# Kernel optimization log

Hardware: AMD Instinct MI355X
Metric: run time of the kernel (lower is better)

## Reference

```python
import jax, jax.numpy as jnp
import numpy as np

B, N, L = 512, 64, 64
D = 256          # item_embed_size / hidden_size
H = 256          # linear_hidden_size
V = 100000       # item_size
STEP = 1


def _p(key, shape, std=0.0625):
    return jax.random.uniform(key, shape, jnp.float32, -std, std)


def setup_inputs() -> dict:
    key = jax.random.key(0)
    ks = jax.random.split(key, 32)
    inp = {
        "alias_inputs": jax.random.randint(ks[0], (B, L), 0, N),
        "A": jax.random.uniform(ks[1], (B, N, 2 * N), jnp.float32),
        "items": jax.random.randint(ks[2], (B, N), 0, V),
        "mask": jnp.ones((B, L), jnp.int32),
        # parameters (stored as [in, out]; torch Linear applies x @ W.T + b)
        "emb": _p(ks[3], (V, D)),
        "W_ein": _p(ks[4], (D, D)), "b_ein": _p(ks[5], (D,)),
        "W_eout": _p(ks[6], (D, D)), "b_eout": _p(ks[7], (D,)),
        "b_iah": _p(ks[8], (D,)), "b_oah": _p(ks[9], (D,)),
        "W_i": _p(ks[10], (2 * D, 3 * D)), "b_i": _p(ks[11], (3 * D,)),
        "W_h": _p(ks[12], (D, 3 * D)), "b_h": _p(ks[13], (3 * D,)),
        "W1": _p(ks[14], (D, D)), "b1": _p(ks[15], (D,)),
        "W2": _p(ks[16], (D, D)), "b2": _p(ks[17], (D,)),
        "W3": _p(ks[18], (D, 1)),
        "Wn1": _p(ks[19], (2 * D, H)), "bn1": _p(ks[20], (H,)),
        "Wn2": _p(ks[21], (H, D)), "bn2": _p(ks[22], (D,)),
    }
    return inp


def reference(alias_inputs, A, items, mask,
              emb, W_ein, b_ein, W_eout, b_eout, b_iah, b_oah,
              W_i, b_i, W_h, b_h, W1, b1, W2, b2, W3, Wn1, bn1, Wn2, bn2):
    n = A.shape[1]
    hidden = emb[items]  # [B, N, D] (dropout is identity at eval)

    def gnn_cell(h):
        inp_in = jnp.matmul(A[:, :, :n], h @ W_ein + b_ein) + b_iah
        inp_out = jnp.matmul(A[:, :, n:2 * n], h @ W_eout + b_eout) + b_oah
        inputs = jnp.concatenate([inp_in, inp_out], axis=2)     # [B, N, 2D]
        gi = inputs @ W_i + b_i                                  # [B, N, 3D]
        gh = h @ W_h + b_h                                       # [B, N, 3D]
        i_r, i_i, i_n = jnp.split(gi, 3, axis=2)
        h_r, h_i, h_n = jnp.split(gh, 3, axis=2)
        resetgate = jax.nn.sigmoid(i_r + h_r)
        inputgate = jax.nn.sigmoid(i_i + h_i)
        newgate = jnp.tanh(i_n + resetgate * h_n)
        return newgate + inputgate * (h - newgate)

    for _ in range(STEP):
        hidden = gnn_cell(hidden)

    # per-sample gather of node states into sequence order
    seq_hidden = jnp.take_along_axis(hidden, alias_inputs[:, :, None], axis=1)  # [B, L, D]
    last = jnp.sum(mask, axis=1) - 1
    ht = seq_hidden[jnp.arange(seq_hidden.shape[0]), last]        # [B, D]

    q1 = (ht @ W1 + b1)[:, None, :]                               # [B, 1, D]
    q2 = seq_hidden @ W2 + b2                                     # [B, L, D]
    alpha = jax.nn.sigmoid(q1 + q2) @ W3                          # [B, L, 1]
    a = jnp.sum(alpha * seq_hidden * mask[:, :, None].astype(jnp.float32), axis=1)  # [B, D]

    x = jnp.concatenate([a, ht], axis=1)                          # [B, 2D]
    return jax.nn.relu(x @ Wn1 + bn1) @ Wn2 + bn2                 # [B, D]
```

## Files before the change

kernel.cpp:

```cpp
#include <hip/hip_runtime.h>
#include <hip/hip_bf16.h>
#include <math.h>

typedef short bhalf8 __attribute__((ext_vector_type(8)));
typedef float floatx4 __attribute__((ext_vector_type(4)));

__device__ __forceinline__ float sigmoidf_(float x) { return 1.0f / (1.0f + __expf(-x)); }

__device__ __forceinline__ unsigned short f2bf(float f) {
    unsigned int u = __builtin_bit_cast(unsigned int, f);
    u += 0x7FFFu + ((u >> 16) & 1u);
    return (unsigned short)(u >> 16);
}
__device__ __forceinline__ float bf2f(unsigned short h) {
    unsigned int u = ((unsigned int)h) << 16;
    return __builtin_bit_cast(float, u);
}

__device__ __forceinline__ floatx4 mfma16(bhalf8 a, bhalf8 b, floatx4 c) {
    return __builtin_amdgcn_mfma_f32_16x16x32_bf16(a, b, c, 0, 0, 0);
}

__device__ __forceinline__ void gl_lds16(const unsigned short* g, unsigned short* l) {
    __builtin_amdgcn_global_load_lds(
        (const __attribute__((address_space(1))) void*)g,
        (__attribute__((address_space(3))) void*)l, 16, 0, 0);
}

__device__ __forceinline__ void pack_generic(
    int b, int tid, const float* __restrict__ W0, const float* __restrict__ W1,
    int split, int N, int BN, unsigned short* __restrict__ out)
{
    int t = b * 256 + tid;
    int j = t & 7;
    int lane = (t >> 3) & 63;
    int FT = BN >> 4;
    int f = (t >> 9) % FT;
    int rest = t / (512 * FT);
    int NT = N / BN;
    int nt = rest % NT;
    int kt = rest / NT;
    int k = kt * 32 + (lane >> 4) * 8 + j;
    int n = nt * BN + f * 16 + (lane & 15);
    float v = (n < split) ? W0[(size_t)k * split + n]
                          : W1[(size_t)k * (N - split) + (n - split)];
    out[t] = f2bf(v);
}

__device__ __forceinline__ void pack_gru_(
    int b, int tid, const float* __restrict__ Wi, const float* __restrict__ Wh,
    unsigned short* __restrict__ out)
{
    int t = b * 256 + tid;
    int j = t & 7;
    int lane = (t >> 3) & 63;
    int f = (t >> 9) & 3;
    int q = t >> 11;
    int g = q % 3;
    int p = q / 3;
    int dt = p & 3;
    int kt = p >> 2;
    int k = kt * 32 + (lane >> 4) * 8 + j;
    int n = g * 256 + dt * 64 + f * 16 + (lane & 15);
    float v = (k < 512) ? Wi[(size_t)k * 768 + n] : Wh[(size_t)(k - 512) * 768 + n];
    out[t] = f2bf(v);
}

__global__ __launch_bounds__(256) void pack_all(
    const float* __restrict__ W_ein, const float* __restrict__ W_eout,
    const float* __restrict__ Wi, const float* __restrict__ Wh,
    const float* __restrict__ W2, const float* __restrict__ Wn1,
    const float* __restrict__ Wn2,
    unsigned short* __restrict__ Wio_pk, unsigned short* __restrict__ Wg_pk,
    unsigned short* __restrict__ W2pk, unsigned short* __restrict__ Wn1pk,
    unsigned short* __restrict__ Wn2pk)
{
    int bx = blockIdx.x;
    int tid = threadIdx.x;
    if (bx < 512)       pack_generic(bx,        tid, W_ein, W_eout, 256, 512, 128, Wio_pk);
    else if (bx < 2816) pack_gru_   (bx - 512,  tid, Wi, Wh, Wg_pk);
    else if (bx < 3072) pack_generic(bx - 2816, tid, W2,  W2,  256, 256, 256, W2pk);
    else if (bx < 3584) pack_generic(bx - 3072, tid, Wn1, Wn1, 256, 256, 256, Wn1pk);
    else                pack_generic(bx - 3584, tid, Wn2, Wn2, 256, 256, 256, Wn2pk);
}

__global__ __launch_bounds__(256) void gather_emb(
    const int* __restrict__ items, const float* __restrict__ emb,
    unsigned short* __restrict__ hidden_pk)
{
    int i = blockIdx.x * 256 + threadIdx.x;
    int mg = i >> 9;
    int rem = i & 511;
    int l = rem & 63;
    int m = mg * 16 + (l & 15);
    int k = (rem >> 6) * 32 + (l >> 4) * 8;
    int it = items[m];
    const float* src = emb + (size_t)it * 256 + k;
    float4 v0 = *(const float4*)src;
    float4 v1 = *(const float4*)(src + 4);
    uint4 o;
    o.x = f2bf(v0.x) | ((unsigned)f2bf(v0.y) << 16);
    o.y = f2bf(v0.z) | ((unsigned)f2bf(v0.w) << 16);
    o.z = f2bf(v1.x) | ((unsigned)f2bf(v1.y) << 16);
    o.w = f2bf(v1.z) | ((unsigned)f2bf(v1.w) << 16);
    *(uint4*)(hidden_pk + (size_t)i * 8) = o;
}

__global__ __launch_bounds__(256) void gemm_hioadj(
    const unsigned short* __restrict__ hidden_pk,
    const unsigned short* __restrict__ Wio_pk,
    const float* __restrict__ bein, const float* __restrict__ beout,
    const float* __restrict__ A,
    const float* __restrict__ biah, const float* __restrict__ boah,
    unsigned short* __restrict__ inp_pk)
{
    __shared__ unsigned short SM[24576];
    unsigned short* As0 = SM;
    unsigned short* Bs0 = SM + 8192;
    unsigned short* Hb  = SM;
    unsigned short* Ab  = SM + 16384;

    const int tid = threadIdx.x;
    const int wid = tid >> 6, lane = tid & 63;
    const int wr = wid >> 1, wc = wid & 1;
    const int bm = blockIdx.x * 128;
    const int nt = blockIdx.y;
    const int mg0 = bm >> 4;
    const int b0 = blockIdx.x * 2;
    const int half = nt >> 1;

    auto stage = [&](int kt, int buf) {
        #pragma unroll
        for (int u = 0; u < 2; ++u) {
            int rg = wid * 2 + u;
            gl_lds16(hidden_pk + ((size_t)(mg0 + rg) * 8 + kt) * 512 + lane * 8,
                     &As0[buf * 4096 + rg * 512]);
            gl_lds16(Wio_pk + ((size_t)(kt * 4 + nt) * 8 + rg) * 512 + lane * 8,
                     &Bs0[buf * 4096 + rg * 512]);
        }
    };

    floatx4 acc[4][4] = {};
    stage(0, 0);
    __syncthreads();
    #pragma unroll
    for (int kt = 0; kt < 8; ++kt) {
        int cur = kt & 1;
        if (kt < 7) stage(kt + 1, cur ^ 1);
        bhalf8 a[4], b[4];
        #pragma unroll
        for (int i = 0; i < 4; i++) a[i] = *(const bhalf8*)&As0[cur * 4096 + (wr * 4 + i) * 512 + lane * 8];
        #pragma unroll
        for (int j = 0; j < 4; j++) b[j] = *(const bhalf8*)&Bs0[cur * 4096 + (wc * 4 + j) * 512 + lane * 8];
        #pragma unroll
        for (int i = 0; i < 4; i++)
            #pragma unroll
            for (int j = 0; j < 4; j++) acc[i][j] = mfma16(a[i], b[j], acc[i][j]);
        __syncthreads();
    }
    const int r0 = (lane >> 4) * 4;
    {
        const float* bio = half ? beout : bein;
        #pragma unroll
        for (int mf = 0; mf < 4; mf++) {
            #pragma unroll
            for (int nf = 0; nf < 4; nf++) {
                int nl = wc * 64 + nf * 16 + (lane & 15);
                float bias = bio[(nt & 1) * 128 + nl];
                int base = (((wr * 2 + (mf >> 1)) * 8 + (nl >> 4)) * 64
                            + ((mf & 1) * 2 + (r0 >> 3)) * 16 + (lane & 15)) * 8 + (r0 & 7);
                ushort4 o;
                o.x = f2bf(acc[mf][nf][0] + bias);
                o.y = f2bf(acc[mf][nf][1] + bias);
                o.z = f2bf(acc[mf][nf][2] + bias);
                o.w = f2bf(acc[mf][nf][3] + bias);
                *(ushort4*)&Hb[base] = o;
            }
        }
    }
    {
        int r = tid >> 2, jj = tid & 3;
        #pragma unroll
        for (int bb = 0; bb < 2; ++bb)
            #pragma unroll
            for (int kt2 = 0; kt2 < 2; ++kt2) {
                const float* src = A + (size_t)(b0 + bb) * 8192 + r * 128 + half * 64 + kt2 * 32 + jj * 8;
                float4 v0 = *(const float4*)src;
                float4 v1 = *(const float4*)(src + 4);
                uint4 o;
                o.x = f2bf(v0.x) | ((unsigned)f2bf(v0.y) << 16);
                o.y = f2bf(v0.z) | ((unsigned)f2bf(v0.w) << 16);
                o.z = f2bf(v1.x) | ((unsigned)f2bf(v1.y) << 16);
                o.w = f2bf(v1.z) | ((unsigned)f2bf(v1.w) << 16);
                *(uint4*)&Ab[(bb * 2 + kt2) * 2048 + ((r >> 4) * 64 + jj * 16 + (r & 15)) * 8] = o;
            }
    }
    __syncthreads();
    const int bb = wid >> 1, ch = wid & 1;
    floatx4 acc2[4][4] = {};
    #pragma unroll
    for (int kt2 = 0; kt2 < 2; ++kt2) {
        bhalf8 a2[4];
        #pragma unroll
        for (int i = 0; i < 4; i++)
            a2[i] = *(const bhalf8*)&Ab[(bb * 2 + kt2) * 2048 + (i * 64 + lane) * 8];
        #pragma unroll
        for (int jf = 0; jf < 4; jf++) {
            bhalf8 bv = *(const bhalf8*)&Hb[((bb * 2 + kt2) * 8 + ch * 4 + jf) * 512 + lane * 8];
            #pragma unroll
            for (int i = 0; i < 4; i++) acc2[i][jf] = mfma16(a2[i], bv, acc2[i][jf]);
        }
    }
    {
        const float* bia = half ? boah : biah;
        const int b = b0 + bb;
        #pragma unroll
        for (int i = 0; i < 4; i++) {
            #pragma unroll
            for (int jf = 0; jf < 4; jf++) {
                int colp = (nt & 1) * 128 + (ch * 4 + jf) * 16 + (lane & 15);
                float bv = bia[colp];
                int kt5 = nt * 4 + ch * 2 + (jf >> 1);
                int l2 = ((jf & 1) * 2 + ((lane >> 3) & 1)) * 16;
                #pragma unroll
                for (int reg = 0; reg < 4; reg++) {
                    int mlo = r0 + reg;
                    size_t dst = (((size_t)(b * 4 + i) * 16 + kt5) * 64 + l2 + mlo) * 8 + (lane & 7);
                    inp_pk[dst] = f2bf(acc2[i][jf][reg] + bv);
                }
            }
        }
    }
}

__global__ __launch_bounds__(256) void gru_mfma(
    const unsigned short* __restrict__ inp_pk,
    const unsigned short* __restrict__ hidden_pk,
    const unsigned short* __restrict__ Wg_pk,
    const float* __restrict__ bi, const float* __restrict__ bh,
    unsigned short* __restrict__ newh_bf)
{
    __shared__ unsigned short As3[3][4096];
    __shared__ unsigned short Bs2[2][6144];
    const int tid = threadIdx.x;
    const int wid = tid >> 6, lane = tid & 63;
    const int wr = wid >> 1, wc = wid & 1;
    const int bm = blockIdx.x * 128;
    const int dt = blockIdx.y;
    const int mg0 = bm >> 4;

    floatx4 R[4][2] = {}, I[4][2] = {}, N0[4][2] = {}, N1[4][2] = {};

    auto stageA = [&](int st, int buf) {
        #pragma unroll
        for (int u = 0; u < 2; ++u) {
            int rg = wid * 2 + u;
            const unsigned short* src = (st < 16)
                ? inp_pk    + ((size_t)(mg0 + rg) * 16 + st) * 512
                : hidden_pk + ((size_t)(mg0 + rg) * 8 + (st - 16)) * 512;
            gl_lds16(src + lane * 8, &As3[buf][rg * 512]);
        }
    };
    auto stageB = [&](int st, int buf) {
        #pragma unroll
        for (int u = 0; u < 3; ++u) {
            int sg = wid * 3 + u;
            gl_lds16(Wg_pk + ((size_t)(st * 4 + dt) * 12 + sg) * 512 + lane * 8,
                     &Bs2[buf][sg * 512]);
        }
    };

    stageA(0, 0);
    stageB(0, 0);
    stageA(1, 1);
    #pragma unroll
    for (int st = 0; st < 24; ++st) {
        const int ca = st % 3, cb = st & 1;
        if (st < 23) asm volatile("s_waitcnt vmcnt(2)" ::: "memory");
        else         asm volatile("s_waitcnt vmcnt(0)" ::: "memory");
        __builtin_amdgcn_s_barrier();
        __builtin_amdgcn_sched_barrier(0);
        if (st < 23) stageB(st + 1, cb ^ 1);
        if (st < 22) stageA(st + 2, (st + 2) % 3);
        bhalf8 a[4];
        #pragma unroll
        for (int i = 0; i < 4; i++)
            a[i] = *(const bhalf8*)&As3[ca][(wr * 4 + i) * 512 + lane * 8];
        #pragma unroll
        for (int f = 0; f < 2; ++f) {
            bhalf8 bv = *(const bhalf8*)&Bs2[cb][(0 * 4 + wc * 2 + f) * 512 + lane * 8];
            #pragma unroll
            for (int i = 0; i < 4; i++) R[i][f] = mfma16(a[i], bv, R[i][f]);
        }
        #pragma unroll
        for (int f = 0; f < 2; ++f) {
            bhalf8 bv = *(const bhalf8*)&Bs2[cb][(1 * 4 + wc * 2 + f) * 512 + lane * 8];
            #pragma unroll
            for (int i = 0; i < 4; i++) I[i][f] = mfma16(a[i], bv, I[i][f]);
        }
        if (st < 16) {
            #pragma unroll
            for (int f = 0; f < 2; ++f) {
                bhalf8 bv = *(const bhalf8*)&Bs2[cb][(2 * 4 + wc * 2 + f) * 512 + lane * 8];
                #pragma unroll
                for (int i = 0; i < 4; i++) N0[i][f] = mfma16(a[i], bv, N0[i][f]);
            }
        } else {
            #pragma unroll
            for (int f = 0; f < 2; ++f) {
                bhalf8 bv = *(const bhalf8*)&Bs2[cb][(2 * 4 + wc * 2 + f) * 512 + lane * 8];
                #pragma unroll
                for (int i = 0; i < 4; i++) N1[i][f] = mfma16(a[i], bv, N1[i][f]);
            }
        }
    }
    const int r0 = (lane >> 4) * 4;
    const int bd = dt * 64 + wc * 32;
    #pragma unroll
    for (int i = 0; i < 4; i++) {
        #pragma unroll
        for (int f = 0; f < 2; f++) {
            int d = bd + f * 16 + (lane & 15);
            float bir = bi[d] + bh[d];
            float bii = bi[256 + d] + bh[256 + d];
            float bin = bi[512 + d];
            float bhn = bh[512 + d];
            #pragma unroll
            for (int reg = 0; reg < 4; reg++) {
                int m = bm + wr * 64 + i * 16 + r0 + reg;
                size_t hidx = (((size_t)(m >> 4) * 8 + (d >> 5)) * 64
                               + ((d >> 3) & 3) * 16 + (m & 15)) * 8 + (d & 7);
                float hv = bf2f(hidden_pk[hidx]);
                float rg = sigmoidf_(R[i][f][reg] + bir);
                float ig = sigmoidf_(I[i][f][reg] + bii);
                float ng = tanhf(N0[i][f][reg] + bin + rg * (N1[i][f][reg] + bhn));
                newh_bf[(size_t)m * 256 + d] = f2bf(ng + ig * (hv - ng));
            }
        }
    }
}

__global__ __launch_bounds__(256) void attn_fused(
    const unsigned short* __restrict__ newh_bf,
    const int* __restrict__ alias, const int* __restrict__ mask,
    const float* __restrict__ W1, const float* __restrict__ b1,
    const float* __restrict__ b2, const float* __restrict__ W3,
    const unsigned short* __restrict__ W2pk,
    unsigned short* __restrict__ ht_bf,
    unsigned short* __restrict__ a_bf)
{
    const int b = blockIdx.x;
    const int tid = threadIdx.x;
    const int wid = tid >> 6, lane = tid & 63;
    __shared__ int arow[64];
    __shared__ int node_s;
    __shared__ float hts[256];
    __shared__ float q1s[256];
    __shared__ float alphap[4][64];
    __shared__ float am[64];
    __shared__ unsigned short As[2048];
    __shared__ unsigned short Bs[8192];
    if (tid < 64) {
        arow[tid] = b * 64 + alias[b * 64 + tid];
        int mv = mask[b * 64 + tid];
        #pragma unroll
        for (int off = 32; off > 0; off >>= 1) mv += __shfl_xor(mv, off);
        if (tid == 0) node_s = b * 64 + alias[b * 64 + (mv - 1)];
    }
    __syncthreads();
    {
        unsigned short hv = newh_bf[(size_t)node_s * 256 + tid];
        ht_bf[(size_t)b * 256 + tid] = hv;
        hts[tid] = bf2f(hv);
    }
    __syncthreads();
    {
        float q0 = 0, q1v = 0, q2v = 0, q3v = 0;
        for (int k = 0; k < 256; k += 4) {
            q0  = fmaf(hts[k],     W1[(size_t)k * 256 + tid],       q0);
            q1v = fmaf(hts[k + 1], W1[(size_t)(k + 1) * 256 + tid], q1v);
            q2v = fmaf(hts[k + 2], W1[(size_t)(k + 2) * 256 + tid], q2v);
            q3v = fmaf(hts[k + 3], W1[(size_t)(k + 3) * 256 + tid], q3v);
        }
        q1s[tid] = (q0 + q1v) + (q2v + q3v) + b1[tid];
    }

    floatx4 acc[4][4] = {};
    #pragma unroll
    for (int kt = 0; kt < 8; ++kt) {
        {
            int r = tid >> 2, jj = tid & 3;
            const unsigned short* src = newh_bf + (size_t)arow[r] * 256 + kt * 32 + jj * 8;
            *(uint4*)&As[((r >> 4) * 64 + jj * 16 + (r & 15)) * 8] = *(const uint4*)src;
        }
        {
            const unsigned short* src = W2pk + (size_t)kt * 16 * 512;
            #pragma unroll
            for (int u = 0; u < 4; ++u) {
                int sg = wid * 4 + u;
                gl_lds16(src + sg * 512 + lane * 8, &Bs[sg * 512]);
            }
        }
        __syncthreads();
        bhalf8 a[4], bb[4];
        #pragma unroll
        for (int i = 0; i < 4; i++) a[i] = *(const bhalf8*)&As[(i * 64 + lane) * 8];
        #pragma unroll
        for (int j = 0; j < 4; j++) bb[j] = *(const bhalf8*)&Bs[((wid * 4 + j) * 64 + lane) * 8];
        #pragma unroll
        for (int i = 0; i < 4; i++)
            #pragma unroll
            for (int j = 0; j < 4; j++) acc[i][j] = mfma16(a[i], bb[j], acc[i][j]);
        __syncthreads();
    }
    float q1v[4], b2v[4], w3v[4];
    #pragma unroll
    for (int j = 0; j < 4; j++) {
        int col = wid * 64 + j * 16 + (lane & 15);
        q1v[j] = q1s[col];
        b2v[j] = b2[col];
        w3v[j] = W3[col];
    }
    #pragma unroll
    for (int i = 0; i < 4; i++) {
        #pragma unroll
        for (int reg = 0; reg < 4; reg++) {
            float t = 0.f;
            #pragma unroll
            for (int j = 0; j < 4; j++)
                t += sigmoidf_(acc[i][j][reg] + q1v[j] + b2v[j]) * w3v[j];
            #pragma unroll
            for (int off = 1; off < 16; off <<= 1) t += __shfl_xor(t, off);
            if ((lane & 15) == 0) alphap[wid][i * 16 + (lane >> 4) * 4 + reg] = t;
        }
    }
    __syncthreads();
    if (tid < 64) {
        float al = alphap[0][tid] + alphap[1][tid] + alphap[2][tid] + alphap[3][tid];
        am[tid] = al * (float)mask[b * 64 + tid];
    }
    __syncthreads();
    float acca = 0.f;
    #pragma unroll 8
    for (int l = 0; l < 64; ++l)
        acca = fmaf(am[l], bf2f(newh_bf[(size_t)arow[l] * 256 + tid]), acca);
    a_bf[(size_t)b * 256 + tid] = f2bf(acca);
}

__global__ __launch_bounds__(256) void mlp_fused(
    const unsigned short* __restrict__ a_bf, const unsigned short* __restrict__ ht_bf,
    const unsigned short* __restrict__ Wn1pk, const float* __restrict__ bn1,
    const unsigned short* __restrict__ Wn2pk, const float* __restrict__ bn2,
    float* __restrict__ out)
{
    __shared__ unsigned short As[4096];
    __shared__ unsigned short Bs[16384];
    __shared__ unsigned short Ys[16384];
    const int tid = threadIdx.x;
    const int wid = tid >> 6, lane = tid & 63;
    const int bm = blockIdx.x * 64;
    const int c = lane & 15;
    const int r0 = (lane >> 4) * 4;

    {
        floatx4 acc[4][4] = {};
        #pragma unroll
        for (int s = 0; s < 8; ++s) {
            #pragma unroll
            for (int v = 0; v < 2; ++v) {
                int kt = s * 2 + v;
                int r = tid >> 2, jj = tid & 3;
                const unsigned short* src = ((kt < 8) ? a_bf : ht_bf)
                    + (size_t)(bm + r) * 256 + (kt & 7) * 32 + jj * 8;
                *(uint4*)&As[v * 2048 + ((r >> 4) * 64 + jj * 16 + (r & 15)) * 8] = *(const uint4*)src;
            }
            #pragma unroll
            for (int u = 0; u < 8; ++u) {
                int sg = wid * 8 + u;
                int ktl = sg >> 4, f = sg & 15;
                gl_lds16(Wn1pk + ((size_t)(s * 2 + ktl) * 16 + f) * 512 + lane * 8, &Bs[sg * 512]);
            }
            __syncthreads();
            #pragma unroll
            for (int v = 0; v < 2; ++v) {
                bhalf8 a[4], bb[4];
                #pragma unroll
                for (int i = 0; i < 4; i++) a[i] = *(const bhalf8*)&As[v * 2048 + (i * 64 + lane) * 8];
                #pragma unroll
                for (int j = 0; j < 4; j++) bb[j] = *(const bhalf8*)&Bs[((v * 16) + wid * 4 + j) * 512 + lane * 8];
                #pragma unroll
                for (int i = 0; i < 4; i++)
                    #pragma unroll
                    for (int j = 0; j < 4; j++) acc[i][j] = mfma16(a[i], bb[j], acc[i][j]);
            }
            __syncthreads();
        }
        #pragma unroll
        for (int i = 0; i < 4; i++) {
            #pragma unroll
            for (int jf = 0; jf < 4; jf++) {
                int n = wid * 64 + jf * 16 + c;
                float bv = bn1[n];
                int kt2 = wid * 2 + (jf >> 1);
                int l2 = ((jf & 1) * 2 + (c >> 3)) * 16;
                #pragma unroll
                for (int reg = 0; reg < 4; reg++) {
                    float v = fmaxf(acc[i][jf][reg] + bv, 0.f);
                    size_t idx = (((size_t)(kt2 * 4 + i) * 64) + l2 + r0 + reg) * 8 + (c & 7);
                    Ys[idx] = f2bf(v);
                }
            }
        }
    }
    __syncthreads();
    floatx4 acc2[4][4] = {};
    #pragma unroll
    for (int s = 0; s < 4; ++s) {
        #pragma unroll
        for (int u = 0; u < 8; ++u) {
            int sg = wid * 8 + u;
            int ktl = sg >> 4, f = sg & 15;
            gl_lds16(Wn2pk + ((size_t)(s * 2 + ktl) * 16 + f) * 512 + lane * 8, &Bs[sg * 512]);
        }
        __syncthreads();
        #pragma unroll
        for (int v = 0; v < 2; ++v) {
            int kt2 = s * 2 + v;
            bhalf8 a[4], bb[4];
            #pragma unroll
            for (int i = 0; i < 4; i++) a[i] = *(const bhalf8*)&Ys[((kt2 * 4 + i) * 64 + lane) * 8];
            #pragma unroll
            for (int j = 0; j < 4; j++) bb[j] = *(const bhalf8*)&Bs[((v * 16) + wid * 4 + j) * 512 + lane * 8];
            #pragma unroll
            for (int i = 0; i < 4; i++)
                #pragma unroll
                for (int j = 0; j < 4; j++) acc2[i][j] = mfma16(a[i], bb[j], acc2[i][j]);
        }
        __syncthreads();
    }
    #pragma unroll
    for (int i = 0; i < 4; i++) {
        #pragma unroll
        for (int jf = 0; jf < 4; jf++) {
            int n = wid * 64 + jf * 16 + c;
            float bv = bn2[n];
            #pragma unroll
            for (int reg = 0; reg < 4; reg++) {
                int m = bm + i * 16 + r0 + reg;
                out[(size_t)m * 256 + n] = acc2[i][jf][reg] + bv;
            }
        }
    }
}

extern "C" void kernel_launch(void* const* d_in, const int* in_sizes, int n_in,
                              void* d_out, int out_size, void* d_ws, size_t ws_size,
                              hipStream_t stream)
{
    const int*   alias  = (const int*)  d_in[0];
    const float* A      = (const float*)d_in[1];
    const int*   items  = (const int*)  d_in[2];
    const int*   mask   = (const int*)  d_in[3];
    const float* emb    = (const float*)d_in[4];
    const float* W_ein  = (const float*)d_in[5];
    const float* b_ein  = (const float*)d_in[6];
    const float* W_eout = (const float*)d_in[7];
    const float* b_eout = (const float*)d_in[8];
    const float* b_iah  = (const float*)d_in[9];
    const float* b_oah  = (const float*)d_in[10];
    const float* W_i    = (const float*)d_in[11];
    const float* b_i    = (const float*)d_in[12];
    const float* W_h    = (const float*)d_in[13];
    const float* b_h    = (const float*)d_in[14];
    const float* W1     = (const float*)d_in[15];
    const float* b1     = (const float*)d_in[16];
    const float* W2     = (const float*)d_in[17];
    const float* b2     = (const float*)d_in[18];
    const float* W3     = (const float*)d_in[19];
    const float* Wn1    = (const float*)d_in[20];
    const float* bn1    = (const float*)d_in[21];
    const float* Wn2    = (const float*)d_in[22];
    const float* bn2    = (const float*)d_in[23];
    float* out = (float*)d_out;
    (void)in_sizes; (void)n_in; (void)out_size; (void)ws_size;

    char* w = (char*)d_ws;
    unsigned short* hidden_pk = (unsigned short*)(w);
    unsigned short* inp_pk    = (unsigned short*)(w + 50331648);
    unsigned short* newh_bf   = (unsigned short*)(w + 83886080);
    unsigned short* Wio_pk    = (unsigned short*)(w + 100663296);
    unsigned short* Wg_pk     = (unsigned short*)(w + 100925440);
    unsigned short* W2pk      = (unsigned short*)(w + 102105088);
    unsigned short* Wn1pk     = (unsigned short*)(w + 102236160);
    unsigned short* Wn2pk     = (unsigned short*)(w + 102498304);
    unsigned short* ht_bf     = (unsigned short*)(w + 102629376);
    unsigned short* a_bf      = (unsigned short*)(w + 102891520);

    pack_all<<<3840, 256, 0, stream>>>(W_ein, W_eout, W_i, W_h, W2, Wn1, Wn2,
                                       Wio_pk, Wg_pk, W2pk, Wn1pk, Wn2pk);
    gather_emb <<<4096, 256, 0, stream>>>(items, emb, hidden_pk);
    gemm_hioadj<<<dim3(256, 4), 256, 0, stream>>>(hidden_pk, Wio_pk, b_ein, b_eout,
                                                  A, b_iah, b_oah, inp_pk);
    gru_mfma   <<<dim3(256, 4), 256, 0, stream>>>(inp_pk, hidden_pk, Wg_pk, b_i, b_h, newh_bf);
    attn_fused <<<512, 256, 0, stream>>>(newh_bf, alias, mask, W1, b1, b2, W3, W2pk, ht_bf, a_bf);
    mlp_fused  <<<8, 256, 0, stream>>>(a_bf, ht_bf, Wn1pk, bn1, Wn2pk, bn2, out);
}
```

Before: 140.4 us.

## Fuse embedding gather into pack kernel and double-buffer attention GEMM staging

Result: no change. 137.7 us (-2.0%).

```diff
diff --git a/kernel.cpp b/kernel.cpp
--- a/kernel.cpp
+++ b/kernel.cpp
@@ -71,39 +71,36 @@
     const float* __restrict__ Wi, const float* __restrict__ Wh,
     const float* __restrict__ W2, const float* __restrict__ Wn1,
     const float* __restrict__ Wn2,
+    const int* __restrict__ items, const float* __restrict__ emb,
     unsigned short* __restrict__ Wio_pk, unsigned short* __restrict__ Wg_pk,
     unsigned short* __restrict__ W2pk, unsigned short* __restrict__ Wn1pk,
-    unsigned short* __restrict__ Wn2pk)
+    unsigned short* __restrict__ Wn2pk, unsigned short* __restrict__ hidden_pk)
 {
     int bx = blockIdx.x;
     int tid = threadIdx.x;
-    if (bx < 512)       pack_generic(bx,        tid, W_ein, W_eout, 256, 512, 128, Wio_pk);
-    else if (bx < 2816) pack_gru_   (bx - 512,  tid, Wi, Wh, Wg_pk);
-    else if (bx < 3072) pack_generic(bx - 2816, tid, W2,  W2,  256, 256, 256, W2pk);
-    else if (bx < 3584) pack_generic(bx - 3072, tid, Wn1, Wn1, 256, 256, 256, Wn1pk);
-    else                pack_generic(bx - 3584, tid, Wn2, Wn2, 256, 256, 256, Wn2pk);
-}
-
-__global__ __launch_bounds__(256) void gather_emb(
-    const int* __restrict__ items, const float* __restrict__ emb,
-    unsigned short* __restrict__ hidden_pk)
-{
-    int i = blockIdx.x * 256 + threadIdx.x;
-    int mg = i >> 9;
-    int rem = i & 511;
-    int l = rem & 63;
-    int m = mg * 16 + (l & 15);
-    int k = (rem >> 6) * 32 + (l >> 4) * 8;
-    int it = items[m];
-    const float* src = emb + (size_t)it * 256 + k;
-    float4 v0 = *(const float4*)src;
-    float4 v1 = *(const float4*)(src + 4);
-    uint4 o;
-    o.x = f2bf(v0.x) | ((unsigned)f2bf(v0.y) << 16);
-    o.y = f2bf(v0.z) | ((unsigned)f2bf(v0.w) << 16);
-    o.z = f2bf(v1.x) | ((unsigned)f2bf(v1.y) << 16);
-    o.w = f2bf(v1.z) | ((unsigned)f2bf(v1.w) << 16);
-    *(uint4*)(hidden_pk + (size_t)i * 8) = o;
+    if (bx < 512)       { pack_generic(bx,        tid, W_ein, W_eout, 256, 512, 128, Wio_pk); return; }
+    if (bx < 2816)      { pack_gru_   (bx - 512,  tid, Wi, Wh, Wg_pk); return; }
+    if (bx < 3072)      { pack_generic(bx - 2816, tid, W2,  W2,  256, 256, 256, W2pk); return; }
+    if (bx < 3584)      { pack_generic(bx - 3072, tid, Wn1, Wn1, 256, 256, 256, Wn1pk); return; }
+    if (bx < 3840)      { pack_generic(bx - 3584, tid, Wn2, Wn2, 256, 256, 256, Wn2pk); return; }
+    {
+        int i = (bx - 3840) * 256 + tid;
+        int mg = i >> 9;
+        int rem = i & 511;
+        int l = rem & 63;
+        int m = mg * 16 + (l & 15);
+        int k = (rem >> 6) * 32 + (l >> 4) * 8;
+        int it = items[m];
+        const float* src = emb + (size_t)it * 256 + k;
+        float4 v0 = *(const float4*)src;
+        float4 v1 = *(const float4*)(src + 4);
+        uint4 o;
+        o.x = f2bf(v0.x) | ((unsigned)f2bf(v0.y) << 16);
+        o.y = f2bf(v0.z) | ((unsigned)f2bf(v0.w) << 16);
+        o.z = f2bf(v1.x) | ((unsigned)f2bf(v1.y) << 16);
+        o.w = f2bf(v1.z) | ((unsigned)f2bf(v1.w) << 16);
+        *(uint4*)(hidden_pk + (size_t)i * 8) = o;
+    }
 }
 
 __global__ __launch_bounds__(256) void gemm_hioadj(
@@ -358,8 +355,8 @@
     __shared__ float q1s[256];
     __shared__ float alphap[4][64];
     __shared__ float am[64];
-    __shared__ unsigned short As[2048];
-    __shared__ unsigned short Bs[8192];
+    __shared__ unsigned short As[2][2048];
+    __shared__ unsigned short Bs[2][8192];
     if (tid < 64) {
         arow[tid] = b * 64 + alias[b * 64 + tid];
         int mv = mask[b * 64 + tid];
@@ -374,6 +371,25 @@
         hts[tid] = bf2f(hv);
     }
     __syncthreads();
+
+    auto stage = [&](int kt, int buf) {
+        {
+            int r = tid >> 2, jj = tid & 3;
+            const unsigned short* src = newh_bf + (size_t)arow[r] * 256 + kt * 32 + jj * 8;
+            *(uint4*)&As[buf][((r >> 4) * 64 + jj * 16 + (r & 15)) * 8] = *(const uint4*)src;
+        }
+        {
+            const unsigned short* src = W2pk + (size_t)kt * 16 * 512;
+            #pragma unroll
+            for (int u = 0; u < 4; ++u) {
+                int sg = wid * 4 + u;
+                gl_lds16(src + sg * 512 + lane * 8, &Bs[buf][sg * 512]);
+            }
+        }
+    };
+
+    floatx4 acc[4][4] = {};
+    stage(0, 0);
     {
         float q0 = 0, q1v = 0, q2v = 0, q3v = 0;
         for (int k = 0; k < 256; k += 4) {
@@ -384,29 +400,16 @@
         }
         q1s[tid] = (q0 + q1v) + (q2v + q3v) + b1[tid];
     }
-
-    floatx4 acc[4][4] = {};
+    __syncthreads();
     #pragma unroll
     for (int kt = 0; kt < 8; ++kt) {
-        {
-            int r = tid >> 2, jj = tid & 3;
-            const unsigned short* src = newh_bf + (size_t)arow[r] * 256 + kt * 32 + jj * 8;
-            *(uint4*)&As[((r >> 4) * 64 + jj * 16 + (r & 15)) * 8] = *(const uint4*)src;
-        }
-        {
-            const unsigned short* src = W2pk + (size_t)kt * 16 * 512;
-            #pragma unroll
-            for (int u = 0; u < 4; ++u) {
-                int sg = wid * 4 + u;
-                gl_lds16(src + sg * 512 + lane * 8, &Bs[sg * 512]);
-            }
-        }
-        __syncthreads();
+        int cur = kt & 1;
+        if (kt < 7) stage(kt + 1, cur ^ 1);
         bhalf8 a[4], bb[4];
         #pragma unroll
-        for (int i = 0; i < 4; i++) a[i] = *(const bhalf8*)&As[(i * 64 + lane) * 8];
-        #pragma unroll
-        for (int j = 0; j < 4; j++) bb[j] = *(const bhalf8*)&Bs[((wid * 4 + j) * 64 + lane) * 8];
+        for (int i = 0; i < 4; i++) a[i] = *(const bhalf8*)&As[cur][(i * 64 + lane) * 8];
+        #pragma unroll
+        for (int j = 0; j < 4; j++) bb[j] = *(const bhalf8*)&Bs[cur][((wid * 4 + j) * 64 + lane) * 8];
         #pragma unroll
         for (int i = 0; i < 4; i++)
             #pragma unroll
@@ -596,9 +599,9 @@
     unsigned short* ht_bf     = (unsigned short*)(w + 102629376);
     unsigned short* a_bf      = (unsigned short*)(w + 102891520);
 
-    pack_all<<<3840, 256, 0, stream>>>(W_ein, W_eout, W_i, W_h, W2, Wn1, Wn2,
-                                       Wio_pk, Wg_pk, W2pk, Wn1pk, Wn2pk);
-    gather_emb <<<4096, 256, 0, stream>>>(items, emb, hidden_pk);
+    pack_all   <<<7936, 256, 0, stream>>>(W_ein, W_eout, W_i, W_h, W2, Wn1, Wn2,
+                                          items, emb,
+                                          Wio_pk, Wg_pk, W2pk, Wn1pk, Wn2pk, hidden_pk);
     gemm_hioadj<<<dim3(256, 4), 256, 0, stream>>>(hidden_pk, Wio_pk, b_ein, b_eout,
                                                   A, b_iah, b_oah, inp_pk);
     gru_mfma   <<<dim3(256, 4), 256, 0, stream>>>(inp_pk, hidden_pk, Wg_pk, b_i, b_h, newh_bf);
```
